# Optimization experiments

Hardware: AMD Instinct MI355X
Metric: run time of the kernel (lower is better)

The kernel has to match this reference:

```python
import jax, jax.numpy as jnp
import numpy as np

N = 50000          # num nodes
E = 800000         # num edges
DIM = 64           # node_channels
EDGE_DIM = 16
HEADS = 4
TIME_STEP = 3
NEG_SLOPE = 0.2
HC = HEADS * DIM


def setup_inputs() -> dict:
    key = jax.random.key(0)
    ks = jax.random.split(key, 16)
    rn = lambda k, shape, s=0.1: (jax.random.normal(k, shape, jnp.float32) * s)
    return {
        "x": jax.random.normal(ks[0], (N, DIM), jnp.float32),
        "edge_index": jax.random.randint(ks[1], (2, E), 0, N, jnp.int32),
        "edge_attr": jax.random.normal(ks[2], (E, EDGE_DIM), jnp.float32),
        "Wn": rn(ks[3], (DIM, HC)),
        "We": rn(ks[4], (EDGE_DIM, HC)),
        "Wa": rn(ks[5], (1, HEADS, 3 * DIM)),
        "Ws": rn(ks[6], (HC, DIM)),
        "b": jnp.zeros((DIM,), jnp.float32),
        "Wih": rn(ks[7], (3 * DIM, DIM)),
        "Whh": rn(ks[8], (3 * DIM, DIM)),
        "bih": rn(ks[9], (3 * DIM,)),
        "bhh": rn(ks[10], (3 * DIM,)),
        "gamma": jnp.ones((DIM,), jnp.float32),
        "beta": jnp.zeros((DIM,), jnp.float32),
    }


def _mhta(x, src, dst, edge_attr, Wn, We, Wa, Ws, b):
    xp = x @ Wn                                    # [N, H*C]
    ep = (edge_attr @ We).reshape(-1, HEADS, DIM)  # [E, H, C]
    x_j = xp[src].reshape(-1, HEADS, DIM)          # source nodes
    x_i = xp[dst].reshape(-1, HEADS, DIM)          # target nodes
    wa = Wa.reshape(HEADS, 3, DIM)                 # split of cat([x_i, e, x_j])
    alpha = (jnp.einsum('ehc,hc->eh', x_i, wa[:, 0])
             + jnp.einsum('ehc,hc->eh', ep, wa[:, 1])
             + jnp.einsum('ehc,hc->eh', x_j, wa[:, 2]))
    alpha = jax.nn.leaky_relu(alpha, NEG_SLOPE)
    # segment softmax grouped by target node (PyG softmax)
    amax = jax.ops.segment_max(alpha, dst, num_segments=N)
    alpha = jnp.exp(alpha - amax[dst])
    denom = jax.ops.segment_sum(alpha, dst, num_segments=N)
    alpha = alpha / (denom[dst] + 1e-16)
    msg = (alpha[:, :, None] * ep * x_j).reshape(-1, HC)
    aggr = jax.ops.segment_sum(msg, dst, num_segments=N)  # [N, H*C]
    return aggr @ Ws + b


def _gru_step(m, h, Wih, Whh, bih, bhh):
    gi = m @ Wih.T + bih
    gh = h @ Whh.T + bhh
    i_r, i_z, i_n = jnp.split(gi, 3, axis=-1)
    h_r, h_z, h_n = jnp.split(gh, 3, axis=-1)
    r = jax.nn.sigmoid(i_r + h_r)
    z = jax.nn.sigmoid(i_z + h_z)
    n = jnp.tanh(i_n + r * h_n)
    return (1.0 - z) * n + z * h


def _layernorm(x, gamma, beta, eps=1e-5):
    mu = jnp.mean(x, axis=-1, keepdims=True)
    var = jnp.mean((x - mu) ** 2, axis=-1, keepdims=True)
    return (x - mu) * jax.lax.rsqrt(var + eps) * gamma + beta


def reference(x, edge_index, edge_attr, Wn, We, Wa, Ws, b,
              Wih, Whh, bih, bhh, gamma, beta):
    src, dst = edge_index[0], edge_index[1]
    h = x  # h0 = x.unsqueeze(0) in torch (seq_len=1 GRU)
    xc = x
    for _ in range(TIME_STEP):
        m = jax.nn.celu(_mhta(xc, src, dst, edge_attr, Wn, We, Wa, Ws, b))
        h = _gru_step(m, h, Wih, Whh, bih, bhh)
        xc = _layernorm(h, gamma, beta)
    return xc
```

## Files before the change

kernel.cpp:

```cpp
#include <hip/hip_runtime.h>
#include <math.h>

#define NNODES 50000
#define NEDGES 800000

typedef _Float16 f16;
typedef _Float16 f16x2 __attribute__((ext_vector_type(2)));
typedef _Float16 f16x4 __attribute__((ext_vector_type(4)));
typedef _Float16 f16x8 __attribute__((ext_vector_type(8)));
typedef float f32x4 __attribute__((ext_vector_type(4)));

#define FMAMIX_LO(ACC, PV, WRD) \
    asm("v_fma_mix_f32 %0, %1, %2, %0 op_sel_hi:[0,1,0]" \
        : "+v"(ACC) : "v"(PV), "v"(WRD))
#define FMAMIX_HI(ACC, PV, WRD) \
    asm("v_fma_mix_f32 %0, %1, %2, %0 op_sel:[0,1,0] op_sel_hi:[0,1,0]" \
        : "+v"(ACC) : "v"(PV), "v"(WRD))

__device__ inline uint pk16(float a, float b) {
    union { f16x2 h; uint u; } c;
    c.h[0] = (f16)a; c.h[1] = (f16)b;
    return c.u;
}
__device__ inline f16x2 bc16(uint u) {
    union { uint u; f16x2 h; } c; c.u = u; return c.h;
}
__device__ inline float wred_max(float v) {
#pragma unroll
    for (int off = 32; off; off >>= 1) v = fmaxf(v, __shfl_xor(v, off, 64));
    return v;
}
__device__ inline float wred_sum(float v) {
#pragma unroll
    for (int off = 32; off; off >>= 1) v += __shfl_xor(v, off, 64);
    return v;
}
__device__ inline float wred_max16(float v) {
#pragma unroll
    for (int off = 8; off; off >>= 1) v = fmaxf(v, __shfl_xor(v, off, 64));
    return v;
}
__device__ inline float wred_sum16(float v) {
#pragma unroll
    for (int off = 8; off; off >>= 1) v += __shfl_xor(v, off, 64);
    return v;
}


__global__ __launch_bounds__(256) void k_fold(
    const float* __restrict__ Wn, const float* __restrict__ We,
    const float* __restrict__ Wa, const float* __restrict__ Wih,
    const float* __restrict__ Whh, const float* __restrict__ Ws,
    float* __restrict__ wnwa0, float* __restrict__ wnwa2,
    float* __restrict__ wewa1, f16* __restrict__ WeB,
    f16* __restrict__ WsP, f16* __restrict__ WihP, f16* __restrict__ WhhP,
    f16* __restrict__ WnB, f16* __restrict__ awB)
{
    int t = threadIdx.x;
    {
        int k = t >> 2, h = t & 3;
        float s0 = 0.f, s2 = 0.f;
        for (int c = 0; c < 64; c++) {
            float wn = Wn[k * 256 + h * 64 + c];
            s0 = fmaf(wn, Wa[h * 192 + c], s0);
            s2 = fmaf(wn, Wa[h * 192 + 128 + c], s2);
        }
        wnwa0[t] = s0;
        wnwa2[t] = s2;
    }
    if (t < 64) {
        int k = t >> 2, h = t & 3;
        float s1 = 0.f;
        for (int c = 0; c < 64; c++)
            s1 = fmaf(We[k * 256 + h * 64 + c], Wa[h * 192 + 64 + c], s1);
        wewa1[t] = s1;
    }
    __syncthreads();
    for (int idx = t; idx < 128; idx += 256) {
        int ks = idx >> 6, l = idx & 63;
        int lg = l >> 4, c = l & 15;
        f16* o = awB + (size_t)idx * 8;
        for (int j = 0; j < 8; j++) {
            int k = ks * 32 + lg * 8 + j;
            float v = (c < 4) ? wnwa0[k * 4 + c] : ((c < 8) ? wnwa2[k * 4 + (c - 4)] : 0.f);
            o[j] = (f16)v;
        }
    }
    for (int idx = t; idx < 2048; idx += 256) {
        int l = idx & 63, tt = (idx >> 6) & 15, ks = idx >> 10;
        int lg = l >> 4, ll = l & 15;
        f16* o = WnB + (size_t)idx * 8;
        for (int j = 0; j < 8; j++)
            o[j] = (f16)Wn[(ks * 32 + lg * 8 + j) * 256 + tt * 16 + ll];
    }
    for (int idx = t; idx < 1024; idx += 256) {
        int tt = idx >> 6, l = idx & 63;
        int lg = l >> 4, ll = l & 15;
        f16* o = WeB + (size_t)idx * 4;
        for (int j = 0; j < 4; j++)
            o[j] = (f16)We[(lg * 4 + j) * 256 + tt * 16 + ll];
    }
    for (int e = t; e < 2048; e += 256) {
        int l = e & 63, tt = (e >> 6) & 3, ks = e >> 8;
        int lg = l >> 4, ll = l & 15;
        f16* o = WsP + (size_t)e * 8;
        for (int j = 0; j < 8; j++)
            o[j] = (f16)Ws[(ks * 32 + lg * 8 + j) * 64 + tt * 16 + ll];
    }
    for (int e = t; e < 1536; e += 256) {
        int l = e & 63, q = e >> 6;
        int tt = q % 12, ks = q / 12;
        int lg = l >> 4, ll = l & 15;
        int outc = tt * 16 + ll;
        for (int j = 0; j < 8; j++) {
            int k = ks * 32 + lg * 8 + j;
            WihP[(size_t)e * 8 + j] = (f16)Wih[outc * 64 + k];
            WhhP[(size_t)e * 8 + j] = (f16)Whh[outc * 64 + k];
        }
    }
}

__global__ __launch_bounds__(256) void k_hist(const int* __restrict__ dst, int* __restrict__ counts)
{
    int e = blockIdx.x * 256 + threadIdx.x;
    atomicAdd(&counts[dst[e]], 1);
}

__global__ __launch_bounds__(1024) void k_scan(const int* __restrict__ counts,
                                               int* __restrict__ row_ptr, int n)
{
    __shared__ int wsum[16];
    int t = threadIdx.x, wid = t >> 6, lane = t & 63;
    int running = 0;
    for (int base = 0; base < n; base += 1024) {
        int idx = base + t;
        int c = (idx < n) ? counts[idx] : 0;
        int v = c;
#pragma unroll
        for (int off = 1; off < 64; off <<= 1) {
            int u = __shfl_up(v, off, 64);
            if (lane >= off) v += u;
        }
        if (lane == 63) wsum[wid] = v;
        __syncthreads();
        int wpre = 0, tot = 0;
#pragma unroll
        for (int wk = 0; wk < 16; wk++) {
            int s = wsum[wk];
            if (wk < wid) wpre += s;
            tot += s;
        }
        if (idx < n) row_ptr[idx] = running + wpre + v - c;
        running += tot;
        __syncthreads();
    }
    if (t == 0) row_ptr[n] = running;
}

__global__ __launch_bounds__(256) void k_scatter(
    const int* __restrict__ srcv, const int* __restrict__ dstv,
    const float* __restrict__ ea, const float* __restrict__ wewa1,
    const int* __restrict__ row_ptr, int* __restrict__ fill,
    int* __restrict__ csr_src, float* __restrict__ ae_csr,
    uint* __restrict__ ea16_csr)
{
    __shared__ float w[64];
    int t = threadIdx.x;
    if (t < 64) w[t] = wewa1[t];
    __syncthreads();
    int e = blockIdx.x * 256 + t;
    int d = dstv[e];
    int pos = row_ptr[d] + atomicAdd(&fill[d], 1);
    csr_src[pos] = srcv[e];
    const float4* p = (const float4*)(ea + (size_t)e * 16);
    float4 v0 = p[0], v1 = p[1], v2 = p[2], v3 = p[3];
    float eav[16] = {v0.x, v0.y, v0.z, v0.w, v1.x, v1.y, v1.z, v1.w,
                     v2.x, v2.y, v2.z, v2.w, v3.x, v3.y, v3.z, v3.w};
    float a0 = 0.f, a1 = 0.f, a2 = 0.f, a3 = 0.f;
#pragma unroll
    for (int k = 0; k < 16; k++) {
        a0 = fmaf(eav[k], w[k * 4 + 0], a0);
        a1 = fmaf(eav[k], w[k * 4 + 1], a1);
        a2 = fmaf(eav[k], w[k * 4 + 2], a2);
        a3 = fmaf(eav[k], w[k * 4 + 3], a3);
    }
    float4 r; r.x = a0; r.y = a1; r.z = a2; r.w = a3;
    *(float4*)(ae_csr + (size_t)pos * 4) = r;
    uint4 pa, pb;
    pa.x = pk16(eav[0], eav[1]);  pa.y = pk16(eav[2], eav[3]);
    pa.z = pk16(eav[4], eav[5]);  pa.w = pk16(eav[6], eav[7]);
    pb.x = pk16(eav[8], eav[9]);  pb.y = pk16(eav[10], eav[11]);
    pb.z = pk16(eav[12], eav[13]); pb.w = pk16(eav[14], eav[15]);
    uint4* d16 = (uint4*)(ea16_csr + (size_t)pos * 8);
    d16[0] = pa; d16[1] = pb;
}


__global__ __launch_bounds__(256) void k_xpaij(
    const float* __restrict__ xc, const f16* __restrict__ WnB,
    const f16* __restrict__ awB, f16* __restrict__ xp16,
    float* __restrict__ aijI, float* __restrict__ aijJ)
{
    int t = threadIdx.x, w = t >> 6, l = t & 63;
    int lg = l >> 4, ll = l & 15;
    int wbase = blockIdx.x * 64 + w * 16;
    int nodeA = wbase + ll;
    int nA = nodeA < NNODES ? nodeA : NNODES - 1;

    f16x8 afr[2];
#pragma unroll
    for (int ks = 0; ks < 2; ks++) {
        const float* xpr = xc + (size_t)nA * 64 + ks * 32 + lg * 8;
        float4 a0 = *(const float4*)xpr;
        float4 a1 = *(const float4*)(xpr + 4);
        f16x8 v;
        v[0] = (f16)a0.x; v[1] = (f16)a0.y; v[2] = (f16)a0.z; v[3] = (f16)a0.w;
        v[4] = (f16)a1.x; v[5] = (f16)a1.y; v[6] = (f16)a1.z; v[7] = (f16)a1.w;
        afr[ks] = v;
    }
    f32x4 zero = {0.f, 0.f, 0.f, 0.f};
    f32x4 c[16];
#pragma unroll
    for (int tt = 0; tt < 16; tt++) c[tt] = zero;
    f32x4 caw = zero;
    const f16x8* WnV = (const f16x8*)WnB;
    const f16x8* awV = (const f16x8*)awB;
#pragma unroll
    for (int ks = 0; ks < 2; ks++) {
        caw = __builtin_amdgcn_mfma_f32_16x16x32_f16(afr[ks], awV[ks * 64 + l], caw, 0, 0, 0);
#pragma unroll
        for (int tt = 0; tt < 16; tt++)
            c[tt] = __builtin_amdgcn_mfma_f32_16x16x32_f16(
                afr[ks], WnV[(ks * 16 + tt) * 64 + l], c[tt], 0, 0, 0);
    }
#pragma unroll
    for (int i = 0; i < 4; i++) {
        int node = wbase + lg * 4 + i;
        if (node < NNODES) {
            f16x8 o0, o1;
#pragma unroll
            for (int tt = 0; tt < 8; tt++) o0[tt] = (f16)c[tt][i];
#pragma unroll
            for (int tt = 0; tt < 8; tt++) o1[tt] = (f16)c[8 + tt][i];
            f16* dstp = xp16 + (size_t)node * 256 + ll * 16;
            *(f16x8*)dstp = o0;
            *(f16x8*)(dstp + 8) = o1;
            if (ll < 4)      aijI[(size_t)node * 4 + ll] = caw[i];
            else if (ll < 8) aijJ[(size_t)node * 4 + (ll - 4)] = caw[i];
        }
    }
}

#define LEAKY(v) ((v) > 0.f ? (v) : 0.2f * (v))

__global__ __launch_bounds__(256) void k_node(
    const int* __restrict__ row_ptr, const int* __restrict__ csr_src,
    const float* __restrict__ ae_csr, const float* __restrict__ aijI,
    const float* __restrict__ aijJ, const f16* __restrict__ xp16,
    const uint* __restrict__ ea16_csr, const f16* __restrict__ WeB,
    f16* __restrict__ aggr16)
{
    __shared__ float wbuf[4][64][4];
    __shared__ uint  eabuf[4][64][8];
    __shared__ int   srcbuf[4][64];
    int t = threadIdx.x, wid = t >> 6, lane = t & 63;
    int ll = lane & 15, g = lane >> 4;
    int n = blockIdx.x * 4 + wid;
    uint4 z4 = {0u, 0u, 0u, 0u};
    *(uint4*)&eabuf[wid][lane][0] = z4;
    *(uint4*)&eabuf[wid][lane][4] = z4;
    f16x4 wb[16];
#pragma unroll
    for (int tt = 0; tt < 16; tt++)
        wb[tt] = *(const f16x4*)(WeB + (size_t)(tt * 64 + lane) * 4);
    int r0 = row_ptr[n], r1 = row_ptr[n + 1];
    int deg = r1 - r0;
    float acc[16];
#pragma unroll
    for (int tt = 0; tt < 16; tt++) acc[tt] = 0.f;
    f32x4 zacc = {0.f, 0.f, 0.f, 0.f};

    auto agg_chunk = [&](int c) {
        int4 s4 = *(const int4*)&srcbuf[wid][c * 16 + g * 4];
        const f16* xr0 = xp16 + ((size_t)(uint)s4.x) * 256 + ll * 16;
        const f16* xr1 = xp16 + ((size_t)(uint)s4.y) * 256 + ll * 16;
        const f16* xr2 = xp16 + ((size_t)(uint)s4.z) * 256 + ll * 16;
        const f16* xr3 = xp16 + ((size_t)(uint)s4.w) * 256 + ll * 16;
        uint4 xA[4], xB[4];
        xA[0] = *(const uint4*)xr0; xB[0] = *(const uint4*)(xr0 + 8);
        xA[1] = *(const uint4*)xr1; xB[1] = *(const uint4*)(xr1 + 8);
        xA[2] = *(const uint4*)xr2; xB[2] = *(const uint4*)(xr2 + 8);
        xA[3] = *(const uint4*)xr3; xB[3] = *(const uint4*)(xr3 + 8);
        f16x4 eaf = *(const f16x4*)((const f16*)&eabuf[wid][c * 16 + ll][0] + g * 4);
        float4 w4 = *(const float4*)&wbuf[wid][c * 16 + ll][0];
        f16 av[4] = {(f16)w4.x, (f16)w4.y, (f16)w4.z, (f16)w4.w};
        f16x4 Ah[4];
#pragma unroll
        for (int h = 0; h < 4; h++)
#pragma unroll
            for (int j = 0; j < 4; j++)
                Ah[h][j] = eaf[j] * av[h];
#pragma unroll
        for (int h = 0; h < 4; h++) {
            f32x4 p0 = __builtin_amdgcn_mfma_f32_16x16x16f16(Ah[h], wb[h * 4 + 0], zacc, 0, 0, 0);
            f32x4 p1 = __builtin_amdgcn_mfma_f32_16x16x16f16(Ah[h], wb[h * 4 + 1], zacc, 0, 0, 0);
            f32x4 p2 = __builtin_amdgcn_mfma_f32_16x16x16f16(Ah[h], wb[h * 4 + 2], zacc, 0, 0, 0);
            f32x4 p3 = __builtin_amdgcn_mfma_f32_16x16x16f16(Ah[h], wb[h * 4 + 3], zacc, 0, 0, 0);
#pragma unroll
            for (int ttl = 0; ttl < 4; ttl++) {
                int tt = h * 4 + ttl;
                f32x4 pv = ttl == 0 ? p0 : (ttl == 1 ? p1 : (ttl == 2 ? p2 : p3));
                int q = tt & 7;
#pragma unroll
                for (int r = 0; r < 4; r++) {
                    uint4 xs = (tt < 8) ? xA[r] : xB[r];
                    uint wrd = (q >> 1) == 0 ? xs.x
                             : ((q >> 1) == 1 ? xs.y : ((q >> 1) == 2 ? xs.z : xs.w));
                    float pvf = pv[r];
                    if (q & 1) FMAMIX_HI(acc[tt], pvf, wrd);
                    else       FMAMIX_LO(acc[tt], pvf, wrd);
                }
            }
        }
    };

    if (deg > 0 && deg <= 64) {
        float4 ai = *(const float4*)(aijI + (size_t)n * 4);
        float al0 = -1e30f, al1 = -1e30f, al2 = -1e30f, al3 = -1e30f;
        int sreg = 0;
        if (lane < deg) {
            int p = r0 + lane;
            sreg = csr_src[p];
            float4 a4 = *(const float4*)(ae_csr + (size_t)p * 4);
            float4 aj = *(const float4*)(aijJ + (size_t)sreg * 4);
            const uint4* ep16 = (const uint4*)(ea16_csr + (size_t)p * 8);
            uint4 ua = ep16[0], ub = ep16[1];
            *(uint4*)&eabuf[wid][lane][0] = ua;
            *(uint4*)&eabuf[wid][lane][4] = ub;
            al0 = LEAKY(ai.x + a4.x + aj.x);
            al1 = LEAKY(ai.y + a4.y + aj.y);
            al2 = LEAKY(ai.z + a4.z + aj.z);
            al3 = LEAKY(ai.w + a4.w + aj.w);
        }
        srcbuf[wid][lane] = (lane < deg) ? sreg : 0;
        float m0, m1, m2, m3, s0, s1, s2, s3;
        float p0, p1, p2, p3;
        if (deg <= 16) {
            m0 = wred_max16(al0); m1 = wred_max16(al1);
            m2 = wred_max16(al2); m3 = wred_max16(al3);
            p0 = (lane < deg) ? __expf(al0 - m0) : 0.f;
            p1 = (lane < deg) ? __expf(al1 - m1) : 0.f;
            p2 = (lane < deg) ? __expf(al2 - m2) : 0.f;
            p3 = (lane < deg) ? __expf(al3 - m3) : 0.f;
            s0 = wred_sum16(p0); s1 = wred_sum16(p1);
            s2 = wred_sum16(p2); s3 = wred_sum16(p3);
        } else {
            m0 = wred_max(al0); m1 = wred_max(al1);
            m2 = wred_max(al2); m3 = wred_max(al3);
            p0 = (lane < deg) ? __expf(al0 - m0) : 0.f;
            p1 = (lane < deg) ? __expf(al1 - m1) : 0.f;
            p2 = (lane < deg) ? __expf(al2 - m2) : 0.f;
            p3 = (lane < deg) ? __expf(al3 - m3) : 0.f;
            s0 = wred_sum(p0); s1 = wred_sum(p1);
            s2 = wred_sum(p2); s3 = wred_sum(p3);
        }
        float4 w4v;
        w4v.x = p0 * (1.f / (s0 + 1e-16f));
        w4v.y = p1 * (1.f / (s1 + 1e-16f));
        w4v.z = p2 * (1.f / (s2 + 1e-16f));
        w4v.w = p3 * (1.f / (s3 + 1e-16f));
        *(float4*)&wbuf[wid][lane][0] = w4v;
        asm volatile("s_waitcnt lgkmcnt(0)" ::: "memory");
        int nch = (deg + 15) >> 4;
        for (int c = 0; c < nch; c++) agg_chunk(c);
    } else if (deg > 0) {
        float4 ai = *(const float4*)(aijI + (size_t)n * 4);
        float m0 = -1e30f, m1 = -1e30f, m2 = -1e30f, m3 = -1e30f;
        float s0 = 0.f, s1 = 0.f, s2 = 0.f, s3 = 0.f;
        for (int base = r0; base < r1; base += 64) {
            int p = base + lane;
            if (p < r1) {
                int s = csr_src[p];
                float4 a4 = *(const float4*)(ae_csr + (size_t)p * 4);
                float4 aj = *(const float4*)(aijJ + (size_t)s * 4);
                float al0 = LEAKY(ai.x + a4.x + aj.x);
                float al1 = LEAKY(ai.y + a4.y + aj.y);
                float al2 = LEAKY(ai.z + a4.z + aj.z);
                float al3 = LEAKY(ai.w + a4.w + aj.w);
                float nm;
                nm = fmaxf(m0, al0); s0 = s0 * __expf(m0 - nm) + __expf(al0 - nm); m0 = nm;
                nm = fmaxf(m1, al1); s1 = s1 * __expf(m1 - nm) + __expf(al1 - nm); m1 = nm;
                nm = fmaxf(m2, al2); s2 = s2 * __expf(m2 - nm) + __expf(al2 - nm); m2 = nm;
                nm = fmaxf(m3, al3); s3 = s3 * __expf(m3 - nm) + __expf(al3 - nm); m3 = nm;
            }
        }
#pragma unroll
        for (int off = 32; off; off >>= 1) {
            float om, os, nm;
            om = __shfl_xor(m0, off, 64); os = __shfl_xor(s0, off, 64);
            nm = fmaxf(m0, om); s0 = s0 * __expf(m0 - nm) + os * __expf(om - nm); m0 = nm;
            om = __shfl_xor(m1, off, 64); os = __shfl_xor(s1, off, 64);
            nm = fmaxf(m1, om); s1 = s1 * __expf(m1 - nm) + os * __expf(om - nm); m1 = nm;
            om = __shfl_xor(m2, off, 64); os = __shfl_xor(s2, off, 64);
            nm = fmaxf(m2, om); s2 = s2 * __expf(m2 - nm) + os * __expf(om - nm); m2 = nm;
            om = __shfl_xor(m3, off, 64); os = __shfl_xor(s3, off, 64);
            nm = fmaxf(m3, om); s3 = s3 * __expf(m3 - nm) + os * __expf(om - nm); m3 = nm;
        }
        float rd0 = 1.f / (s0 + 1e-16f), rd1 = 1.f / (s1 + 1e-16f);
        float rd2 = 1.f / (s2 + 1e-16f), rd3 = 1.f / (s3 + 1e-16f);
        for (int base = r0; base < r1; base += 64) {
            int cnt = min(64, r1 - base);
            float4 w4v = {0.f, 0.f, 0.f, 0.f};
            int sreg = 0;
            if (lane < cnt) {
                int p = base + lane;
                sreg = csr_src[p];
                float4 a4 = *(const float4*)(ae_csr + (size_t)p * 4);
                float4 aj = *(const float4*)(aijJ + (size_t)sreg * 4);
                const uint4* ep16 = (const uint4*)(ea16_csr + (size_t)p * 8);
                uint4 ua = ep16[0], ub = ep16[1];
                *(uint4*)&eabuf[wid][lane][0] = ua;
                *(uint4*)&eabuf[wid][lane][4] = ub;
                float al0 = LEAKY(ai.x + a4.x + aj.x);
                float al1 = LEAKY(ai.y + a4.y + aj.y);
                float al2 = LEAKY(ai.z + a4.z + aj.z);
                float al3 = LEAKY(ai.w + a4.w + aj.w);
                w4v.x = __expf(al0 - m0) * rd0;
                w4v.y = __expf(al1 - m1) * rd1;
                w4v.z = __expf(al2 - m2) * rd2;
                w4v.w = __expf(al3 - m3) * rd3;
            } else {
                *(uint4*)&eabuf[wid][lane][0] = z4;
                *(uint4*)&eabuf[wid][lane][4] = z4;
            }
            *(float4*)&wbuf[wid][lane][0] = w4v;
            srcbuf[wid][lane] = (lane < cnt) ? sreg : 0;
            asm volatile("s_waitcnt lgkmcnt(0)" ::: "memory");
            int nch = (cnt + 15) >> 4;
            for (int c = 0; c < nch; c++) agg_chunk(c);
            asm volatile("s_waitcnt lgkmcnt(0)" ::: "memory");
        }
    }
#pragma unroll
    for (int tt = 0; tt < 16; tt++) {
        float v = acc[tt];
        v += __shfl_xor(v, 16, 64);
        v += __shfl_xor(v, 32, 64);
        acc[tt] = v;
    }
    f16* ag = aggr16 + (size_t)n * 256;
#pragma unroll
    for (int tt = 0; tt < 16; tt++)
        if ((tt >> 2) == g) ag[tt * 16 + ll] = (f16)acc[tt];
}

__global__ __launch_bounds__(256) void k_post(
    const f16* __restrict__ aggr16, const f16* __restrict__ WsP,
    const float* __restrict__ bvec, const float* __restrict__ h_in,
    float* __restrict__ h_out, const f16* __restrict__ WihP,
    const f16* __restrict__ WhhP, const float* __restrict__ bih,
    const float* __restrict__ bhh, const float* __restrict__ gamma,
    const float* __restrict__ beta, float* __restrict__ xc_out)
{
    __shared__ __align__(16) f16 m_lds[4][16][72];
    int t = threadIdx.x, w = t >> 6, l = t & 63;
    int lg = l >> 4, ll = l & 15;
    int nb = blockIdx.x * 64 + w * 16;
    int nodeA = nb + ll;
    int nodeAc = nodeA < NNODES ? nodeA : NNODES - 1;

    f32x4 zero = {0.f, 0.f, 0.f, 0.f};
    f32x4 acc1[4];
#pragma unroll
    for (int tt = 0; tt < 4; tt++) acc1[tt] = zero;
    const f16x8* WsV = (const f16x8*)WsP;
#pragma unroll
    for (int ks = 0; ks < 8; ks++) {
        f16x8 a = *(const f16x8*)(aggr16 + (size_t)nodeAc * 256 + ks * 32 + lg * 8);
#pragma unroll
        for (int tt = 0; tt < 4; tt++) {
            f16x8 b = WsV[(ks * 4 + tt) * 64 + l];
            acc1[tt] = __builtin_amdgcn_mfma_f32_16x16x32_f16(a, b, acc1[tt], 0, 0, 0);
        }
    }
#pragma unroll
    for (int tt = 0; tt < 4; tt++) {
        float bj = bvec[tt * 16 + ll];
#pragma unroll
        for (int i = 0; i < 4; i++) {
            float v = acc1[tt][i] + bj;
            v = v > 0.f ? v : (__expf(v) - 1.f);
            m_lds[w][lg * 4 + i][tt * 16 + ll] = (f16)v;
        }
    }
    asm volatile("s_waitcnt lgkmcnt(0)" ::: "memory");

    f16x8 mf[2], hf[2];
#pragma unroll
    for (int ks = 0; ks < 2; ks++) {
        mf[ks] = *(const f16x8*)(&m_lds[w][ll][ks * 32 + lg * 8]);
        const float* hp = h_in + (size_t)nodeAc * 64 + ks * 32 + lg * 8;
        float4 h0 = *(const float4*)(hp);
        float4 h1 = *(const float4*)(hp + 4);
        f16x8 hh;
        hh[0] = (f16)h0.x; hh[1] = (f16)h0.y; hh[2] = (f16)h0.z; hh[3] = (f16)h0.w;
        hh[4] = (f16)h1.x; hh[5] = (f16)h1.y; hh[6] = (f16)h1.z; hh[7] = (f16)h1.w;
        hf[ks] = hh;
    }
    f32x4 accI[12], accH[12];
#pragma unroll
    for (int tt = 0; tt < 12; tt++) { accI[tt] = zero; accH[tt] = zero; }
    const f16x8* WiV = (const f16x8*)WihP;
    const f16x8* WhV = (const f16x8*)WhhP;
#pragma unroll
    for (int ks = 0; ks < 2; ks++) {
#pragma unroll
        for (int tt = 0; tt < 12; tt++) {
            f16x8 bi = WiV[(ks * 12 + tt) * 64 + l];
            accI[tt] = __builtin_amdgcn_mfma_f32_16x16x32_f16(mf[ks], bi, accI[tt], 0, 0, 0);
            f16x8 bh = WhV[(ks * 12 + tt) * 64 + l];
            accH[tt] = __builtin_amdgcn_mfma_f32_16x16x32_f16(hf[ks], bh, accH[tt], 0, 0, 0);
        }
    }

    float bI[12], bH[12];
#pragma unroll
    for (int tt = 0; tt < 12; tt++) {
        bI[tt] = bih[ll + 16 * tt];
        bH[tt] = bhh[ll + 16 * tt];
    }
    float ga[4], be[4];
#pragma unroll
    for (int u = 0; u < 4; u++) { ga[u] = gamma[ll + 16 * u]; be[u] = beta[ll + 16 * u]; }
    float hnew[4][4];
#pragma unroll
    for (int i = 0; i < 4; i++) {
        int node = nb + lg * 4 + i;
        int nc = node < NNODES ? node : NNODES - 1;
        const float* hrow = h_in + (size_t)nc * 64 + ll;
#pragma unroll
        for (int u = 0; u < 4; u++) {
            float hv = hrow[16 * u];
            float r = 1.f / (1.f + __expf(-(accI[u][i] + bI[u] + accH[u][i] + bH[u])));
            float z = 1.f / (1.f + __expf(-(accI[u + 4][i] + bI[u + 4] + accH[u + 4][i] + bH[u + 4])));
            float pre = accI[u + 8][i] + bI[u + 8] + r * (accH[u + 8][i] + bH[u + 8]);
            float e2 = __expf(2.f * pre);
            float nn = 1.f - 2.f / (e2 + 1.f);
            hnew[i][u] = (1.f - z) * nn + z * hv;
        }
    }
#pragma unroll
    for (int i = 0; i < 4; i++) {
        float s = hnew[i][0] + hnew[i][1] + hnew[i][2] + hnew[i][3];
        float q = hnew[i][0] * hnew[i][0] + hnew[i][1] * hnew[i][1]
                + hnew[i][2] * hnew[i][2] + hnew[i][3] * hnew[i][3];
#pragma unroll
        for (int off = 1; off < 16; off <<= 1) {
            s += __shfl_xor(s, off, 64);
            q += __shfl_xor(q, off, 64);
        }
        float mu = s * (1.f / 64.f);
        float var = q * (1.f / 64.f) - mu * mu;
        float rstd = rsqrtf(var + 1e-5f);
        int node = nb + lg * 4 + i;
        if (node < NNODES) {
            float* ho = h_out + (size_t)node * 64 + ll;
            float* xo = xc_out + (size_t)node * 64 + ll;
#pragma unroll
            for (int u = 0; u < 4; u++) {
                ho[16 * u] = hnew[i][u];
                xo[16 * u] = (hnew[i][u] - mu) * rstd * ga[u] + be[u];
            }
        }
    }
}


extern "C" void kernel_launch(void* const* d_in, const int* in_sizes, int n_in,
                              void* d_out, int out_size, void* d_ws, size_t ws_size,
                              hipStream_t stream)
{
    const float* x         = (const float*)d_in[0];
    const int*   edge_index= (const int*)d_in[1];
    const float* edge_attr = (const float*)d_in[2];
    const float* Wn        = (const float*)d_in[3];
    const float* We        = (const float*)d_in[4];
    const float* Wa        = (const float*)d_in[5];
    const float* Ws        = (const float*)d_in[6];
    const float* bv        = (const float*)d_in[7];
    const float* Wih       = (const float*)d_in[8];
    const float* Whh       = (const float*)d_in[9];
    const float* bih       = (const float*)d_in[10];
    const float* bhh       = (const float*)d_in[11];
    const float* gamma     = (const float*)d_in[12];
    const float* beta      = (const float*)d_in[13];
    float* out = (float*)d_out;

    const int* src = edge_index;
    const int* dst = edge_index + NEDGES;

    char* w = (char*)d_ws;
    auto alloc = [&](size_t bytes) {
        char* p = w;
        w += (bytes + 255) & ~(size_t)255;
        return p;
    };
    f16*   xp16     = (f16*)alloc((size_t)NNODES * 256 * 2);
    f16*   aggr16   = (f16*)alloc((size_t)NNODES * 256 * 2);
    float* ae_csr   = (float*)alloc((size_t)NEDGES * 4 * 4);
    uint*  ea16_csr = (uint*)alloc((size_t)NEDGES * 8 * 4);
    float* hbuf     = (float*)alloc((size_t)NNODES * 64 * 4);
    float* aijI     = (float*)alloc((size_t)NNODES * 4 * 4);
    float* aijJ     = (float*)alloc((size_t)NNODES * 4 * 4);
    int*   counts   = (int*)alloc((size_t)NNODES * 4);
    int*   fill     = (int*)alloc((size_t)NNODES * 4);
    int*   row_ptr  = (int*)alloc((size_t)(NNODES + 1) * 4);
    int*   csr_src  = (int*)alloc((size_t)NEDGES * 4);
    float* wnwa0    = (float*)alloc(256 * 4);
    float* wnwa2    = (float*)alloc(256 * 4);
    float* wewa1    = (float*)alloc(64 * 4);
    f16*   WeB      = (f16*)alloc(1024 * 4 * 2);
    f16*   WsP      = (f16*)alloc(2048 * 8 * 2);
    f16*   WihP     = (f16*)alloc(1536 * 8 * 2);
    f16*   WhhP     = (f16*)alloc(1536 * 8 * 2);
    f16*   WnB      = (f16*)alloc(2048 * 8 * 2);
    f16*   awB      = (f16*)alloc(128 * 8 * 2);

    k_fold<<<1, 256, 0, stream>>>(Wn, We, Wa, Wih, Whh, Ws, wnwa0, wnwa2, wewa1,
                                  WeB, WsP, WihP, WhhP, WnB, awB);
    hipMemsetAsync(counts, 0, (size_t)NNODES * 4, stream);
    hipMemsetAsync(fill, 0, (size_t)NNODES * 4, stream);
    k_hist<<<NEDGES / 256, 256, 0, stream>>>(dst, counts);
    k_scan<<<1, 1024, 0, stream>>>(counts, row_ptr, NNODES);
    k_scatter<<<NEDGES / 256, 256, 0, stream>>>(src, dst, edge_attr, wewa1,
                                                row_ptr, fill, csr_src,
                                                ae_csr, ea16_csr);

    for (int step = 0; step < 3; step++) {
        const float* xc_in = (step == 0) ? x : out;
        const float* h_in  = (step == 0) ? x : hbuf;
        k_xpaij<<<(NNODES + 63) / 64, 256, 0, stream>>>(xc_in, WnB, awB,
                                                        xp16, aijI, aijJ);
        k_node<<<NNODES / 4, 256, 0, stream>>>(row_ptr, csr_src, ae_csr, aijI,
                                               aijJ, xp16, ea16_csr, WeB, aggr16);
        k_post<<<(NNODES + 63) / 64, 256, 0, stream>>>(
            aggr16, WsP, bv, h_in, hbuf, WihP, WhhP, bih, bhh, gamma, beta, out);
    }
}
```

Baseline: 579.5 us.

## Sort nodes by in-degree bucket so waves in a block have balanced work

Adds a per-call counting sort of nodes by in-degree (clamped at 64) to build a permutation, and k_node now processes nodes in that order. Grouping similar-degree nodes into the same block is meant to reduce wave divergence and tail imbalance, where a block waits on its highest-degree wave. It costs three small extra kernels plus memsets, and it loses the locality of writing aggr16 rows in node order.

```diff
diff --git a/kernel.cpp b/kernel.cpp
--- a/kernel.cpp
+++ b/kernel.cpp
@@ -155,6 +155,38 @@
         __syncthreads();
     }
     if (t == 0) row_ptr[n] = running;
+}
+
+__global__ __launch_bounds__(256) void k_bhist(const int* __restrict__ counts,
+                                               int* __restrict__ bcount)
+{
+    int n = blockIdx.x * 256 + threadIdx.x;
+    if (n < NNODES) {
+        int d = counts[n];
+        atomicAdd(&bcount[d > 64 ? 64 : d], 1);
+    }
+}
+
+__global__ __launch_bounds__(64) void k_bscan(const int* __restrict__ bcount,
+                                              int* __restrict__ boff)
+{
+    if (threadIdx.x == 0) {
+        int run = 0;
+        for (int b = 0; b < 65; b++) { boff[b] = run; run += bcount[b]; }
+    }
+}
+
+__global__ __launch_bounds__(256) void k_bscatter(
+    const int* __restrict__ counts, const int* __restrict__ boff,
+    int* __restrict__ bfill, int* __restrict__ perm)
+{
+    int n = blockIdx.x * 256 + threadIdx.x;
+    if (n < NNODES) {
+        int d = counts[n];
+        int b = d > 64 ? 64 : d;
+        int pos = boff[b] + atomicAdd(&bfill[b], 1);
+        perm[pos] = n;
+    }
 }
 
 __global__ __launch_bounds__(256) void k_scatter(
@@ -258,14 +290,14 @@
     const float* __restrict__ ae_csr, const float* __restrict__ aijI,
     const float* __restrict__ aijJ, const f16* __restrict__ xp16,
     const uint* __restrict__ ea16_csr, const f16* __restrict__ WeB,
-    f16* __restrict__ aggr16)
+    const int* __restrict__ perm, f16* __restrict__ aggr16)
 {
     __shared__ float wbuf[4][64][4];
     __shared__ uint  eabuf[4][64][8];
     __shared__ int   srcbuf[4][64];
     int t = threadIdx.x, wid = t >> 6, lane = t & 63;
     int ll = lane & 15, g = lane >> 4;
-    int n = blockIdx.x * 4 + wid;
+    int n = perm[blockIdx.x * 4 + wid];
     uint4 z4 = {0u, 0u, 0u, 0u};
     *(uint4*)&eabuf[wid][lane][0] = z4;
     *(uint4*)&eabuf[wid][lane][4] = z4;
@@ -616,6 +648,10 @@
     int*   fill     = (int*)alloc((size_t)NNODES * 4);
     int*   row_ptr  = (int*)alloc((size_t)(NNODES + 1) * 4);
     int*   csr_src  = (int*)alloc((size_t)NEDGES * 4);
+    int*   perm     = (int*)alloc((size_t)NNODES * 4);
+    int*   bcount   = (int*)alloc(65 * 4);
+    int*   boff     = (int*)alloc(65 * 4);
+    int*   bfill    = (int*)alloc(65 * 4);
     float* wnwa0    = (float*)alloc(256 * 4);
     float* wnwa2    = (float*)alloc(256 * 4);
     float* wewa1    = (float*)alloc(64 * 4);
@@ -630,8 +666,13 @@
                                   WeB, WsP, WihP, WhhP, WnB, awB);
     hipMemsetAsync(counts, 0, (size_t)NNODES * 4, stream);
     hipMemsetAsync(fill, 0, (size_t)NNODES * 4, stream);
+    hipMemsetAsync(bcount, 0, 65 * 4, stream);
+    hipMemsetAsync(bfill, 0, 65 * 4, stream);
     k_hist<<<NEDGES / 256, 256, 0, stream>>>(dst, counts);
     k_scan<<<1, 1024, 0, stream>>>(counts, row_ptr, NNODES);
+    k_bhist<<<(NNODES + 255) / 256, 256, 0, stream>>>(counts, bcount);
+    k_bscan<<<1, 64, 0, stream>>>(bcount, boff);
+    k_bscatter<<<(NNODES + 255) / 256, 256, 0, stream>>>(counts, boff, bfill, perm);
     k_scatter<<<NEDGES / 256, 256, 0, stream>>>(src, dst, edge_attr, wewa1,
                                                 row_ptr, fill, csr_src,
                                                 ae_csr, ea16_csr);
@@ -642,7 +683,8 @@
         k_xpaij<<<(NNODES + 63) / 64, 256, 0, stream>>>(xc_in, WnB, awB,
                                                         xp16, aijI, aijJ);
         k_node<<<NNODES / 4, 256, 0, stream>>>(row_ptr, csr_src, ae_csr, aijI,
-                                               aijJ, xp16, ea16_csr, WeB, aggr16);
+                                               aijJ, xp16, ea16_csr, WeB, perm,
+                                               aggr16);
         k_post<<<(NNODES + 63) / 64, 256, 0, stream>>>(
             aggr16, WsP, bv, h_in, hbuf, WihP, WhhP, bih, bhh, gamma, beta, out);
     }
```

New measurement: 849.9 us. +46.7%, slower.
